# Kernel optimization log

Measured on AMD Instinct MI355X. Metric: run time of the kernel, lower is better.

## Reference

```python
import jax, jax.numpy as jnp
import numpy as np

GROUPS = 32
EPS = 1e-6


def group_norm(x, gamma, beta):
    b, c, h, w = x.shape
    xg = x.reshape(b, GROUPS, c // GROUPS, h, w)
    mu = xg.mean(axis=(2, 3, 4), keepdims=True)
    var = xg.var(axis=(2, 3, 4), keepdims=True)
    xn = ((xg - mu) * jax.lax.rsqrt(var + EPS)).reshape(b, c, h, w)
    return xn * gamma[None, :, None, None] + beta[None, :, None, None]


def conv1x1(x, w, b):
    # x: (b,c_in,h,w), w: (c_out,c_in), b: (c_out,)
    return jnp.einsum('oc,bchw->bohw', w, x) + b[None, :, None, None]


def setup_inputs() -> dict:
    key = jax.random.key(0)
    ks = jax.random.split(key, 10)
    c = 512
    scale = 1.0 / np.sqrt(c)
    inp = jax.random.normal(ks[0], (16, c, 32, 32), dtype=jnp.float32)
    return {
        'inp': inp,
        'gamma': jnp.ones((c,), jnp.float32),
        'beta': jnp.zeros((c,), jnp.float32),
        'Wq': jax.random.normal(ks[1], (c, c), jnp.float32) * scale,
        'bq': jnp.zeros((c,), jnp.float32),
        'Wk': jax.random.normal(ks[2], (c, c), jnp.float32) * scale,
        'bk': jnp.zeros((c,), jnp.float32),
        'Wv': jax.random.normal(ks[3], (c, c), jnp.float32) * scale,
        'bv': jnp.zeros((c,), jnp.float32),
        'Wo': jax.random.normal(ks[4], (c, c), jnp.float32) * scale,
        'bo': jnp.zeros((c,), jnp.float32),
    }


def reference(inp, gamma, beta, Wq, bq, Wk, bk, Wv, bv, Wo, bo):
    b, c, h, w = inp.shape
    x = group_norm(inp, gamma, beta)
    Q = conv1x1(x, Wq, bq).reshape(b, c, h * w)  # (b,c,n)
    K = conv1x1(x, Wk, bk).reshape(b, c, h * w)  # (b,c,m)
    V = conv1x1(x, Wv, bv).reshape(b, c, h * w)  # (b,c,m)
    # attn[b,n,m] = sum_c Q[b,c,n] * K[b,c,m], scaled then softmax over m
    attn = jnp.einsum('bcn,bcm->bnm', Q, K) / jnp.sqrt(jnp.float32(c))
    attn = jax.nn.softmax(attn, axis=2)
    # A[b,c,n] = sum_m V[b,c,m] * attn[b,n,m]  (== bmm(V, attn^T))
    A = jnp.einsum('bcm,bnm->bcn', V, attn).reshape(b, c, h, w)
    A = conv1x1(A, Wo, bo)
    return inp + A
```

## Files before the change

### kernel.cpp

```cpp
#include <hip/hip_runtime.h>

typedef unsigned short UST;
typedef __attribute__((ext_vector_type(8))) short bf16x8;
typedef __attribute__((ext_vector_type(8))) unsigned short us8;
typedef __attribute__((ext_vector_type(4))) float f32x4;

__device__ __forceinline__ UST f2bf(float f) {
  union { float f; unsigned int u; } x; x.f = f;
  unsigned int r = x.u + 0x7fffu + ((x.u >> 16) & 1u);
  return (UST)(r >> 16);
}
__device__ __forceinline__ float bf2f(UST h) {
  union { unsigned int u; float f; } x; x.u = ((unsigned int)h) << 16;
  return x.f;
}

__device__ __forceinline__ void sync_lds() {
  asm volatile("s_waitcnt lgkmcnt(0)\n\ts_barrier" ::: "memory");
}
__device__ __forceinline__ void barrier_nowait() {
  asm volatile("s_barrier" ::: "memory");
}

__global__ __launch_bounds__(256) void prep(
    const float* __restrict__ inp, const float* __restrict__ gamma,
    const float* __restrict__ beta, UST* __restrict__ Xnt,
    const float4* __restrict__ wq, const float4* __restrict__ wk,
    const float4* __restrict__ wv, const float4* __restrict__ wo,
    ushort4* __restrict__ oqkv, ushort4* __restrict__ owo,
    const float4* __restrict__ bq4, const float4* __restrict__ bk4,
    const float4* __restrict__ bv4, float4* __restrict__ bqkv4) {
  const int tid = threadIdx.x;
  if (blockIdx.x >= 512) {
    const int wb = blockIdx.x - 512;
    int i = wb * 256 + tid;
    float4 v;
    v = wq[i]; oqkv[i]          = make_ushort4(f2bf(v.x), f2bf(v.y), f2bf(v.z), f2bf(v.w));
    v = wk[i]; oqkv[i + 65536]  = make_ushort4(f2bf(v.x), f2bf(v.y), f2bf(v.z), f2bf(v.w));
    v = wv[i]; oqkv[i + 131072] = make_ushort4(f2bf(v.x), f2bf(v.y), f2bf(v.z), f2bf(v.w));
    v = wo[i]; owo[i]           = make_ushort4(f2bf(v.x), f2bf(v.y), f2bf(v.z), f2bf(v.w));
    if (wb < 2) {
      int t = wb * 256 + tid;
      if (t < 384) bqkv4[t] = (t < 128) ? bq4[t] : (t < 256 ? bk4[t - 128] : bv4[t - 256]);
    }
    return;
  }
  const int g = blockIdx.x & 31, b = blockIdx.x >> 5;
  const float* base = inp + ((size_t)b * 32 + g) * 16384;
  const float4* p4 = (const float4*)base;
  float s = 0.f, ss = 0.f;
#pragma unroll
  for (int i = 0; i < 16; i++) {
    float4 t = p4[tid + i * 256];
    s += t.x + t.y + t.z + t.w;
    ss += t.x * t.x + t.y * t.y + t.z * t.z + t.w * t.w;
  }
  for (int o = 32; o >= 1; o >>= 1) { s += __shfl_xor(s, o); ss += __shfl_xor(ss, o); }
  __shared__ float red[8];
  __shared__ float mu_s, rstd_s;
  const int w = tid >> 6;
  if ((tid & 63) == 0) { red[w * 2] = s; red[w * 2 + 1] = ss; }
  __syncthreads();
  if (tid == 0) {
    float S1 = red[0] + red[2] + red[4] + red[6];
    float S2 = red[1] + red[3] + red[5] + red[7];
    float mu = S1 * (1.f / 16384.f);
    float var = S2 * (1.f / 16384.f) - mu * mu;
    mu_s = mu; rstd_s = rsqrtf(var + 1e-6f);
  }
  __syncthreads();
  const float mu = mu_s, rstd = rstd_s;
#pragma unroll
  for (int cc = 0; cc < 2; cc++) {
    const int ccg = g * 2 + cc;
    float sc[8], sh[8];
#pragma unroll
    for (int j = 0; j < 8; j++) {
      int ch = ccg * 8 + j;
      sc[j] = gamma[ch] * rstd;
      sh[j] = beta[ch] - mu * sc[j];
    }
#pragma unroll
    for (int i = 0; i < 4; i++) {
      const int n = tid + i * 256;
      us8 v;
#pragma unroll
      for (int j = 0; j < 8; j++) {
        float x = inp[((size_t)b * 512 + ccg * 8 + j) * 1024 + n];
        v[j] = f2bf(x * sc[j] + sh[j]);
      }
      *(us8*)(Xnt + (size_t)b * 524288 + (size_t)ccg * 8192 + (size_t)n * 8) = v;
    }
  }
}

__global__ __launch_bounds__(256) void softmax_k(const UST* __restrict__ S,
                                                 UST* __restrict__ P) {
  const int w = threadIdx.x >> 6, lane = threadIdx.x & 63;
  const size_t row = (size_t)blockIdx.x * 4 + w;
  const us8* Sr = (const us8*)(S + row * 1024);
  us8 a = Sr[lane], b = Sr[64 + lane];
  float v[16];
#pragma unroll
  for (int j = 0; j < 8; j++) { v[j] = bf2f(a[j]); v[8 + j] = bf2f(b[j]); }
  float m = v[0];
#pragma unroll
  for (int i = 1; i < 16; i++) m = fmaxf(m, v[i]);
#pragma unroll
  for (int o = 32; o >= 1; o >>= 1) m = fmaxf(m, __shfl_xor(m, o));
  float s = 0.f;
#pragma unroll
  for (int i = 0; i < 16; i++) { v[i] = __expf(v[i] - m); s += v[i]; }
#pragma unroll
  for (int o = 32; o >= 1; o >>= 1) s += __shfl_xor(s, o);
  const float rs = 1.f / s;
  us8* Pr = (us8*)(P + row * 1024);
  us8 oa, ob;
#pragma unroll
  for (int j = 0; j < 8; j++) { oa[j] = f2bf(v[j] * rs); ob[j] = f2bf(v[8 + j] * rs); }
  Pr[lane] = oa; Pr[64 + lane] = ob;
}

template <int EPI, bool SWZ>
__global__ __launch_bounds__(256, 2) void gemm_bt(
    const UST* __restrict__ A, const UST* __restrict__ B, void* __restrict__ C,
    const float* __restrict__ bias, const float* __restrict__ extra, float scale,
    int K, int ldc,
    int rsA, int csA, int ssA, int rsB, int csB, int ssB,
    long zA, long zB, long zC) {
  __shared__ __align__(16) UST buf[20480];
  UST* l0A = buf;
  UST* l0B = buf + 5120;
  UST* l1A = buf + 10240;
  UST* l1B = buf + 15360;

  const int tid = threadIdx.x;
  int m0, n0, z;
  if constexpr (SWZ) {
    int lin = blockIdx.x + 12 * (blockIdx.y + 8 * blockIdx.z);
    int g = lin & 7, idx = lin >> 3;
    int al = idx / 12, x = idx - al * 12;
    int at = g * 16 + al;
    m0 = (at & 7) * 128; n0 = x * 128; z = at >> 3;
  } else {
    m0 = blockIdx.y * 128; n0 = blockIdx.x * 128; z = blockIdx.z;
  }
  const UST* Ab = A + (long)z * zA;
  const UST* Bb = B + (long)z * zB;

  const int w = tid >> 6, lane = tid & 63;
  const int quad = lane >> 4, l16 = lane & 15;
  const int wm = w >> 1, wn = w & 1;

  f32x4 acc[4][4];
#pragma unroll
  for (int i = 0; i < 4; i++)
#pragma unroll
    for (int j = 0; j < 4; j++) acc[i][j] = f32x4{0.f, 0.f, 0.f, 0.f};

  const int rowa = tid >> 2;
  const int kchunk = tid & 3;
  const UST* gA = Ab + (size_t)(m0 + rowa) * rsA + (size_t)kchunk * csA;
  const UST* gB = Bb + (size_t)(n0 + rowa) * rsB + (size_t)kchunk * csB;
  const size_t a64 = (size_t)64 * rsA, b64 = (size_t)64 * rsB;
  const int lw = rowa * 40 + kchunk * 8;

  const int nk = K >> 5;

  us8 pa0 = *(const us8*)gA, pa1 = *(const us8*)(gA + a64);
  us8 pb0 = *(const us8*)gB, pb1 = *(const us8*)(gB + b64);
  *(us8*)(l0A + lw) = pa0; *(us8*)(l0A + lw + 2560) = pa1;
  *(us8*)(l0B + lw) = pb0; *(us8*)(l0B + lw + 2560) = pb1;
  if (nk > 1) {
    gA += ssA; gB += ssB;
    pa0 = *(const us8*)gA; pa1 = *(const us8*)(gA + a64);
    pb0 = *(const us8*)gB; pb1 = *(const us8*)(gB + b64);
  }
  sync_lds();

  for (int k = 0; k < nk; ++k) {
    UST* curA = (k & 1) ? l1A : l0A;
    UST* curB = (k & 1) ? l1B : l0B;
    UST* nxtA = (k & 1) ? l0A : l1A;
    UST* nxtB = (k & 1) ? l0B : l1B;
    if (k + 1 < nk) {
      *(us8*)(nxtA + lw) = pa0; *(us8*)(nxtA + lw + 2560) = pa1;
      *(us8*)(nxtB + lw) = pb0; *(us8*)(nxtB + lw + 2560) = pb1;
    }
    us8 qa0, qa1, qb0, qb1;
    if (k + 2 < nk) {
      gA += ssA; gB += ssB;
      qa0 = *(const us8*)gA; qa1 = *(const us8*)(gA + a64);
      qb0 = *(const us8*)gB; qb1 = *(const us8*)(gB + b64);
    }
    bf16x8 af[4], bfr[4];
#pragma unroll
    for (int i = 0; i < 4; i++)
      af[i] = *(const bf16x8*)(curA + (wm * 64 + i * 16 + l16) * 40 + quad * 8);
#pragma unroll
    for (int j = 0; j < 4; j++)
      bfr[j] = *(const bf16x8*)(curB + (wn * 64 + j * 16 + l16) * 40 + quad * 8);
#pragma unroll
    for (int i = 0; i < 4; i++)
#pragma unroll
      for (int j = 0; j < 4; j++)
        acc[i][j] = __builtin_amdgcn_mfma_f32_16x16x32_bf16(af[i], bfr[j], acc[i][j], 0, 0, 0);
    sync_lds();
    pa0 = qa0; pa1 = qa1; pb0 = qb0; pb1 = qb1;
  }

  if constexpr (EPI == 4) {
    float* fbuf = (float*)buf;
    float* Cb = (float*)C + (long)z * zC;
    const float* Eb = extra + (long)z * zC;
#pragma unroll
    for (int p = 0; p < 4; ++p) {
      if (p) barrier_nowait();
      if (wm == (p >> 1)) {
#pragma unroll
        for (int ii = 0; ii < 2; ii++) {
          const int i = (p & 1) * 2 + ii;
#pragma unroll
          for (int j = 0; j < 4; j++)
#pragma unroll
            for (int r = 0; r < 4; r++)
              fbuf[(ii * 16 + quad * 4 + r) * 132 + wn * 64 + j * 16 + l16] = acc[i][j][r];
        }
      }
      sync_lds();
#pragma unroll
      for (int it = 0; it < 4; ++it) {
        int q = tid + it * 256;
        int row = q >> 5, colc = q & 31;
        int gr = m0 + p * 32 + row;
        size_t off = (size_t)gr * ldc + n0 + colc * 4;
        float4 v = *(float4*)&fbuf[row * 132 + colc * 4];
        float4 e = *(const float4*)&Eb[off];
        float bb = bias[gr];
        v.x += bb + e.x; v.y += bb + e.y; v.z += bb + e.z; v.w += bb + e.w;
        *(float4*)&Cb[off] = v;
      }
    }
  } else {
    const bool vreg = (EPI == 6) && (n0 >= 1024);
    if (!vreg) {
      UST* Cb = (UST*)C + (long)z * zC;
#pragma unroll
      for (int h = 0; h < 2; ++h) {
        if (h) barrier_nowait();
        if (wm == h) {
#pragma unroll
          for (int i = 0; i < 4; i++)
#pragma unroll
            for (int j = 0; j < 4; j++) {
              float bc = 0.f;
              if constexpr (EPI == 6) bc = bias[n0 + wn * 64 + j * 16 + l16];
#pragma unroll
              for (int r = 0; r < 4; r++) {
                float v = acc[i][j][r] + bc;
                if constexpr (EPI == 5) v *= scale;
                buf[(i * 16 + quad * 4 + r) * 136 + wn * 64 + j * 16 + l16] = f2bf(v);
              }
            }
        }
        sync_lds();
#pragma unroll
        for (int it = 0; it < 4; ++it) {
          int q = tid + it * 256;
          int row = q >> 4, colc = q & 15;
          us8 v = *(us8*)&buf[row * 136 + colc * 8];
          *(us8*)&Cb[(size_t)(m0 + h * 64 + row) * ldc + n0 + colc * 8] = v;
        }
      }
    } else {
      UST* Vb = (UST*)extra + (long)z * 524288;
#pragma unroll
      for (int h = 0; h < 2; ++h) {
        if (h) barrier_nowait();
        if (wn == h) {
#pragma unroll
          for (int i = 0; i < 4; i++)
#pragma unroll
            for (int j = 0; j < 4; j++) {
              const float bc = bias[n0 + wn * 64 + j * 16 + l16];
#pragma unroll
              for (int r = 0; r < 4; r++) {
                float v = acc[i][j][r] + bc;
                buf[(j * 16 + l16) * 136 + wm * 64 + i * 16 + quad * 4 + r] = f2bf(v);
              }
            }
        }
        sync_lds();
#pragma unroll
        for (int it = 0; it < 4; ++it) {
          int q = tid + it * 256;
          int c = q >> 4, mc = q & 15;
          us8 v = *(us8*)&buf[c * 136 + mc * 8];
          *(us8*)&Vb[(size_t)(n0 - 1024 + h * 64 + c) * 1024 + m0 + mc * 8] = v;
        }
      }
    }
  }
}

extern "C" void kernel_launch(void* const* d_in, const int* in_sizes, int n_in,
                              void* d_out, int out_size, void* d_ws, size_t ws_size,
                              hipStream_t stream) {
  const float* inp   = (const float*)d_in[0];
  const float* gamma = (const float*)d_in[1];
  const float* beta  = (const float*)d_in[2];
  const float* Wq    = (const float*)d_in[3];
  const float* bq    = (const float*)d_in[4];
  const float* Wk    = (const float*)d_in[5];
  const float* bk    = (const float*)d_in[6];
  const float* Wv    = (const float*)d_in[7];
  const float* bv    = (const float*)d_in[8];
  const float* Wo    = (const float*)d_in[9];
  const float* bo    = (const float*)d_in[10];
  float* out = (float*)d_out;
  char* ws = (char*)d_ws;

  UST*   Xnt   = (UST*)(ws);
  UST*   QKt   = (UST*)(ws + ((size_t)16 << 20));
  UST*   V     = (UST*)(ws + ((size_t)48 << 20));
  UST*   S     = (UST*)(ws + ((size_t)64 << 20));
  float* bqkv  = (float*)(ws + ((size_t)96 << 20));
  UST*   Wqkvb = (UST*)(ws + ((size_t)96 << 20) + 8192);
  UST*   Wob   = Wqkvb + 786432;
  UST*   P     = QKt;
  UST*   At    = Xnt;

  prep<<<768, 256, 0, stream>>>(
      inp, gamma, beta, Xnt,
      (const float4*)Wq, (const float4*)Wk, (const float4*)Wv, (const float4*)Wo,
      (ushort4*)Wqkvb, (ushort4*)Wob,
      (const float4*)bq, (const float4*)bk, (const float4*)bv, (float4*)bqkv);

  gemm_bt<6, true><<<dim3(12, 8, 16), 256, 0, stream>>>(
      Xnt, Wqkvb, QKt, bqkv, (const float*)V, 1.f,
      512, 1024, 8, 8192, 32768, 512, 8, 32, 524288, 0, 1048576);
  gemm_bt<5, false><<<dim3(8, 8, 16), 256, 0, stream>>>(
      QKt, QKt + 512, S, nullptr, nullptr, 0.04419417382415922f,
      512, 1024, 1024, 8, 32, 1024, 8, 32, 1048576, 1048576, 1048576);
  softmax_k<<<4096, 256, 0, stream>>>(S, P);
  gemm_bt<3, false><<<dim3(4, 8, 16), 256, 0, stream>>>(
      P, V, At, nullptr, nullptr, 1.f,
      1024, 512, 1024, 8, 32, 1024, 8, 32, 1048576, 524288, 524288);
  gemm_bt<4, false><<<dim3(8, 4, 16), 256, 0, stream>>>(
      Wob, At, out, bo, inp, 1.f,
      512, 1024, 512, 8, 32, 512, 8, 32, 0, 524288, 524288);
}
```

Baseline: 240.5 us.

## Fuse softmax into QK^T and PV GEMM epilogues with atomic row sums

Drops the separate softmax kernel. The QK^T GEMM epilogue now writes exp(score*scale) as bf16 and atomically adds per-row sums into a float buffer that the prep kernel zeroes. The PV GEMM epilogue divides by those row sums. This removes a full read and write of the 16x1024x1024 score matrix and one launch, but there is no max subtraction, so it relies on the scores being small enough not to overflow exp. The swizzled block scheduling is also generalized and applied to all GEMMs.

After: 224.3 us. 1.07x faster.

```diff
diff --git a/kernel.cpp b/kernel.cpp
--- a/kernel.cpp
+++ b/kernel.cpp
@@ -29,8 +29,14 @@
     const float4* __restrict__ wv, const float4* __restrict__ wo,
     ushort4* __restrict__ oqkv, ushort4* __restrict__ owo,
     const float4* __restrict__ bq4, const float4* __restrict__ bk4,
-    const float4* __restrict__ bv4, float4* __restrict__ bqkv4) {
+    const float4* __restrict__ bv4, float4* __restrict__ bqkv4,
+    float4* __restrict__ l4) {
   const int tid = threadIdx.x;
+  if (blockIdx.x >= 768) {
+    int i = (blockIdx.x - 768) * 256 + tid;
+    l4[i] = make_float4(0.f, 0.f, 0.f, 0.f);
+    return;
+  }
   if (blockIdx.x >= 512) {
     const int wb = blockIdx.x - 512;
     int i = wb * 256 + tid;
@@ -94,34 +100,7 @@
   }
 }
 
-__global__ __launch_bounds__(256) void softmax_k(const UST* __restrict__ S,
-                                                 UST* __restrict__ P) {
-  const int w = threadIdx.x >> 6, lane = threadIdx.x & 63;
-  const size_t row = (size_t)blockIdx.x * 4 + w;
-  const us8* Sr = (const us8*)(S + row * 1024);
-  us8 a = Sr[lane], b = Sr[64 + lane];
-  float v[16];
-#pragma unroll
-  for (int j = 0; j < 8; j++) { v[j] = bf2f(a[j]); v[8 + j] = bf2f(b[j]); }
-  float m = v[0];
-#pragma unroll
-  for (int i = 1; i < 16; i++) m = fmaxf(m, v[i]);
-#pragma unroll
-  for (int o = 32; o >= 1; o >>= 1) m = fmaxf(m, __shfl_xor(m, o));
-  float s = 0.f;
-#pragma unroll
-  for (int i = 0; i < 16; i++) { v[i] = __expf(v[i] - m); s += v[i]; }
-#pragma unroll
-  for (int o = 32; o >= 1; o >>= 1) s += __shfl_xor(s, o);
-  const float rs = 1.f / s;
-  us8* Pr = (us8*)(P + row * 1024);
-  us8 oa, ob;
-#pragma unroll
-  for (int j = 0; j < 8; j++) { oa[j] = f2bf(v[j] * rs); ob[j] = f2bf(v[8 + j] * rs); }
-  Pr[lane] = oa; Pr[64 + lane] = ob;
-}
-
-template <int EPI, bool SWZ>
+template <int EPI, int NT>
 __global__ __launch_bounds__(256, 2) void gemm_bt(
     const UST* __restrict__ A, const UST* __restrict__ B, void* __restrict__ C,
     const float* __restrict__ bias, const float* __restrict__ extra, float scale,
@@ -136,12 +115,14 @@
 
   const int tid = threadIdx.x;
   int m0, n0, z;
-  if constexpr (SWZ) {
-    int lin = blockIdx.x + 12 * (blockIdx.y + 8 * blockIdx.z);
+  if constexpr (NT > 0) {
+    int lin = blockIdx.x + NT * (blockIdx.y + gridDim.y * blockIdx.z);
+    int T = gridDim.y * gridDim.z;
+    int per = T >> 3;
     int g = lin & 7, idx = lin >> 3;
-    int al = idx / 12, x = idx - al * 12;
-    int at = g * 16 + al;
-    m0 = (at & 7) * 128; n0 = x * 128; z = at >> 3;
+    int at = g * per + idx / NT;
+    int x = idx % NT;
+    m0 = (at % gridDim.y) * 128; z = at / gridDim.y; n0 = x * 128;
   } else {
     m0 = blockIdx.y * 128; n0 = blockIdx.x * 128; z = blockIdx.z;
   }
@@ -241,8 +222,70 @@
         *(float4*)&Cb[off] = v;
       }
     }
+  } else if constexpr (EPI == 7) {
+    UST* Cb = (UST*)C + (long)z * zC;
+    float* lrow = (float*)extra + (long)z * 1024;
+#pragma unroll
+    for (int h = 0; h < 2; ++h) {
+      if (h) barrier_nowait();
+      if (wm == h) {
+#pragma unroll
+        for (int i = 0; i < 4; i++)
+#pragma unroll
+          for (int j = 0; j < 4; j++)
+#pragma unroll
+            for (int r = 0; r < 4; r++) {
+              float v = __expf(acc[i][j][r] * scale);
+              buf[(i * 16 + quad * 4 + r) * 136 + wn * 64 + j * 16 + l16] = f2bf(v);
+            }
+      }
+      sync_lds();
+#pragma unroll
+      for (int it = 0; it < 4; ++it) {
+        int q = tid + it * 256;
+        int row = q >> 4, colc = q & 15;
+        us8 v = *(us8*)&buf[row * 136 + colc * 8];
+        *(us8*)&Cb[(size_t)(m0 + h * 64 + row) * ldc + n0 + colc * 8] = v;
+        float s = 0.f;
+#pragma unroll
+        for (int j = 0; j < 8; j++) s += bf2f(v[j]);
+        s += __shfl_xor(s, 8); s += __shfl_xor(s, 4);
+        s += __shfl_xor(s, 2); s += __shfl_xor(s, 1);
+        if ((lane & 15) == 0) atomicAdd(&lrow[m0 + h * 64 + row], s);
+      }
+    }
+  } else if constexpr (EPI == 8) {
+    UST* Cb = (UST*)C + (long)z * zC;
+    const float* lrow = bias + (long)z * 1024;
+#pragma unroll
+    for (int h = 0; h < 2; ++h) {
+      if (h) barrier_nowait();
+      if (wm == h) {
+#pragma unroll
+        for (int i = 0; i < 4; i++) {
+          float rs[4];
+#pragma unroll
+          for (int r = 0; r < 4; r++)
+            rs[r] = 1.0f / lrow[m0 + h * 64 + i * 16 + quad * 4 + r];
+#pragma unroll
+          for (int j = 0; j < 4; j++)
+#pragma unroll
+            for (int r = 0; r < 4; r++)
+              buf[(i * 16 + quad * 4 + r) * 136 + wn * 64 + j * 16 + l16] =
+                  f2bf(acc[i][j][r] * rs[r]);
+        }
+      }
+      sync_lds();
+#pragma unroll
+      for (int it = 0; it < 4; ++it) {
+        int q = tid + it * 256;
+        int row = q >> 4, colc = q & 15;
+        us8 v = *(us8*)&buf[row * 136 + colc * 8];
+        *(us8*)&Cb[(size_t)(m0 + h * 64 + row) * ldc + n0 + colc * 8] = v;
+      }
+    }
   } else {
-    const bool vreg = (EPI == 6) && (n0 >= 1024);
+    const bool vreg = (n0 >= 1024);
     if (!vreg) {
       UST* Cb = (UST*)C + (long)z * zC;
 #pragma unroll
@@ -253,14 +296,11 @@
           for (int i = 0; i < 4; i++)
 #pragma unroll
             for (int j = 0; j < 4; j++) {
-              float bc = 0.f;
-              if constexpr (EPI == 6) bc = bias[n0 + wn * 64 + j * 16 + l16];
-#pragma unroll
-              for (int r = 0; r < 4; r++) {
-                float v = acc[i][j][r] + bc;
-                if constexpr (EPI == 5) v *= scale;
-                buf[(i * 16 + quad * 4 + r) * 136 + wn * 64 + j * 16 + l16] = f2bf(v);
-              }
+              const float bc = bias[n0 + wn * 64 + j * 16 + l16];
+#pragma unroll
+              for (int r = 0; r < 4; r++)
+                buf[(i * 16 + quad * 4 + r) * 136 + wn * 64 + j * 16 + l16] =
+                    f2bf(acc[i][j][r] + bc);
             }
         }
         sync_lds();
@@ -284,10 +324,9 @@
             for (int j = 0; j < 4; j++) {
               const float bc = bias[n0 + wn * 64 + j * 16 + l16];
 #pragma unroll
-              for (int r = 0; r < 4; r++) {
-                float v = acc[i][j][r] + bc;
-                buf[(j * 16 + l16) * 136 + wm * 64 + i * 16 + quad * 4 + r] = f2bf(v);
-              }
+              for (int r = 0; r < 4; r++)
+                buf[(j * 16 + l16) * 136 + wm * 64 + i * 16 + quad * 4 + r] =
+                    f2bf(acc[i][j][r] + bc);
             }
         }
         sync_lds();
@@ -323,30 +362,30 @@
   UST*   Xnt   = (UST*)(ws);
   UST*   QKt   = (UST*)(ws + ((size_t)16 << 20));
   UST*   V     = (UST*)(ws + ((size_t)48 << 20));
-  UST*   S     = (UST*)(ws + ((size_t)64 << 20));
+  UST*   P     = (UST*)(ws + ((size_t)64 << 20));
   float* bqkv  = (float*)(ws + ((size_t)96 << 20));
   UST*   Wqkvb = (UST*)(ws + ((size_t)96 << 20) + 8192);
   UST*   Wob   = Wqkvb + 786432;
-  UST*   P     = QKt;
+  float* l     = (float*)(ws + ((size_t)100 << 20));
   UST*   At    = Xnt;
 
-  prep<<<768, 256, 0, stream>>>(
+  prep<<<784, 256, 0, stream>>>(
       inp, gamma, beta, Xnt,
       (const float4*)Wq, (const float4*)Wk, (const float4*)Wv, (const float4*)Wo,
       (ushort4*)Wqkvb, (ushort4*)Wob,
-      (const float4*)bq, (const float4*)bk, (const float4*)bv, (float4*)bqkv);
-
-  gemm_bt<6, true><<<dim3(12, 8, 16), 256, 0, stream>>>(
+      (const float4*)bq, (const float4*)bk, (const float4*)bv, (float4*)bqkv,
+      (float4*)l);
+
+  gemm_bt<6, 12><<<dim3(12, 8, 16), 256, 0, stream>>>(
       Xnt, Wqkvb, QKt, bqkv, (const float*)V, 1.f,
       512, 1024, 8, 8192, 32768, 512, 8, 32, 524288, 0, 1048576);
-  gemm_bt<5, false><<<dim3(8, 8, 16), 256, 0, stream>>>(
-      QKt, QKt + 512, S, nullptr, nullptr, 0.04419417382415922f,
+  gemm_bt<7, 8><<<dim3(8, 8, 16), 256, 0, stream>>>(
+      QKt, QKt + 512, P, nullptr, (const float*)l, 0.04419417382415922f,
       512, 1024, 1024, 8, 32, 1024, 8, 32, 1048576, 1048576, 1048576);
-  softmax_k<<<4096, 256, 0, stream>>>(S, P);
-  gemm_bt<3, false><<<dim3(4, 8, 16), 256, 0, stream>>>(
-      P, V, At, nullptr, nullptr, 1.f,
+  gemm_bt<8, 4><<<dim3(4, 8, 16), 256, 0, stream>>>(
+      P, V, At, (const float*)l, nullptr, 1.f,
       1024, 512, 1024, 8, 32, 1024, 8, 32, 1048576, 524288, 524288);
-  gemm_bt<4, false><<<dim3(8, 4, 16), 256, 0, stream>>>(
+  gemm_bt<4, 8><<<dim3(8, 4, 16), 256, 0, stream>>>(
       Wob, At, out, bo, inp, 1.f,
       512, 1024, 512, 8, 32, 512, 8, 32, 0, 524288, 524288);
 }
```
